# Kernel tuning notes

Hardware: AMD Instinct MI355X
Metric: run time of the kernel (lower is better)

The kernel has to match this reference:

```python
import jax, jax.numpy as jnp
import numpy as np

N_SAMPLES = 4194304
N_RAYS = 131072


def setup_inputs() -> dict:
    key = jax.random.key(0)
    k1, k2, k3, k4, k5, k6 = jax.random.split(key, 6)
    alpha = jax.random.uniform(k1, (N_SAMPLES, 1), dtype=jnp.float32)
    values3d = jax.random.uniform(k2, (N_SAMPLES, 3), dtype=jnp.float32)
    values1d = jax.random.uniform(k3, (N_SAMPLES, 1), dtype=jnp.float32)
    weights = jax.random.uniform(k4, (N_SAMPLES, 1), dtype=jnp.float32)
    sample_values = jax.random.normal(k5, (N_SAMPLES, 3), dtype=jnp.float32)
    ray_id = jnp.sort(jax.random.randint(k6, (N_SAMPLES,), 0, N_RAYS, dtype=jnp.int32))
    return {"alpha": alpha, "values3d": values3d, "values1d": values1d,
            "weights": weights, "sample_values": sample_values,
            "ray_id": ray_id, "n_rays": N_RAYS}


def _transmittance(alpha, ray_id, n_rays):
    # exclusive cumprod of (1 - alpha) within each packed ray segment, in log space
    logs = jnp.log(jnp.clip(1.0 - alpha[:, 0], 1e-7, 1.0))          # [N]
    csum = jnp.cumsum(logs)
    excl = csum - logs                                               # exclusive cumsum
    first = jnp.concatenate([jnp.ones((1,), bool), ray_id[1:] != ray_id[:-1]])
    seg_base = jax.ops.segment_sum(jnp.where(first, excl, 0.0), ray_id,
                                   num_segments=n_rays)              # [R]
    transmittance = jnp.exp(excl - seg_base[ray_id])[:, None]        # [N,1]
    bg_transmittance = jnp.exp(jax.ops.segment_sum(logs, ray_id,
                                                   num_segments=n_rays))  # [R]
    return transmittance, bg_transmittance


def reference(alpha, values3d, values1d, weights, sample_values, ray_id, n_rays):
    transmittance, bg_transmittance = _transmittance(alpha, ray_id, n_rays)
    # integrate_3d / integrate_1d: per-ray sum of value * weight
    integrated_3d = jax.ops.segment_sum(values3d * weights, ray_id, num_segments=n_rays)  # [R,3]
    integrated_1d = jax.ops.segment_sum(values1d * weights, ray_id, num_segments=n_rays)  # [R,1]
    # SumOverRay: per-ray sum plus broadcast back to each sample
    sum_per_ray = jax.ops.segment_sum(sample_values, ray_id, num_segments=n_rays)         # [R,3]
    sum_per_sample = sum_per_ray[ray_id]                                                  # [N,3]
    return (transmittance, bg_transmittance, integrated_3d, integrated_1d,
            sum_per_ray, sum_per_sample)
```

## Files before the change

### kernel.cpp

```cpp
#include <hip/hip_runtime.h>

typedef float f32x4 __attribute__((ext_vector_type(4)));

template<int CTRL>
__device__ __forceinline__ float dpp1(float x) {
    return __int_as_float(__builtin_amdgcn_update_dpp(
        0x3f800000, __float_as_int(x), CTRL, 0xF, 0xF, false));
}
template<int CTRL>
__device__ __forceinline__ float dpp0(float x) {
    return __int_as_float(__builtin_amdgcn_update_dpp(
        0, __float_as_int(x), CTRL, 0xF, 0xF, true));
}
template<int PAT>
__device__ __forceinline__ float swz(float x) {
    return __int_as_float(__builtin_amdgcn_ds_swizzle(__float_as_int(x), PAT));
}
#define FUNNEL16(v) do { \
    v += dpp0<0x111>(v); \
    v += dpp0<0x112>(v); \
    v += dpp0<0x114>(v); \
    v += dpp0<0x118>(v); } while (0)

__device__ __forceinline__ void ntst4(float* p, float x, float y, float z, float w) {
    f32x4 v = {x, y, z, w};
    __builtin_nontemporal_store(v, (f32x4*)p);
}

__global__ __launch_bounds__(256) void seg_bounds_kernel(
    const int* __restrict__ ray_id, int n, int* __restrict__ seg_se)
{
    const int t = blockIdx.x * blockDim.x + threadIdx.x;
    const int a = t * 4;
    if (a >= n) return;
    const int4 rv = *(const int4*)(ray_id + a);
    const int prev = (a == 0) ? -1 : ray_id[a - 1];
    const int nxt  = (a + 4 < n) ? ray_id[a + 4] : -1;

    if (rv.x != prev) seg_se[2 * rv.x] = a;
    if (rv.y != rv.x) { seg_se[2 * rv.x + 1] = a + 1; seg_se[2 * rv.y] = a + 1; }
    if (rv.z != rv.y) { seg_se[2 * rv.y + 1] = a + 2; seg_se[2 * rv.z] = a + 2; }
    if (rv.w != rv.z) { seg_se[2 * rv.z + 1] = a + 3; seg_se[2 * rv.w] = a + 3; }
    if (rv.w != nxt)  seg_se[2 * rv.w + 1] = a + 4;
}

__global__ __launch_bounds__(256) void ray_kernel(
    const float* __restrict__ alpha,
    const float* __restrict__ values3d,
    const float* __restrict__ values1d,
    const float* __restrict__ weights,
    const float* __restrict__ sample_values,
    const int*   __restrict__ ray_id,
    const int*   __restrict__ seg_se,
    float* __restrict__ out_T,
    float* __restrict__ out_bg,
    float* __restrict__ out_i3,
    float* __restrict__ out_i1,
    float* __restrict__ out_spr,
    float* __restrict__ out_sps,
    int R, int N)
{
    __shared__ float prr[16][8];

    const int lane = threadIdx.x & 63;
    const int wid  = threadIdx.x >> 6;
    const int j    = lane & 15;
    const int g    = lane >> 4;
    const int slot = wid * 4 + g;
    const int r0   = blockIdx.x * 16;
    const int r    = r0 + slot;
    const bool ray_ok = (r < R);
    const int rc = ray_ok ? r : 0;

    const int2 se = ((const int2*)seg_se)[rc];
    int s0 = se.x, s1 = se.y;
    const bool arith = ray_ok & (s0 >= 0) & (s0 < s1) & (s1 <= N);
    if (!arith) { s0 = 0; s1 = 0; }

    const int chk = ray_id[s0];
    const bool valid = arith & (chk == rc);

    float c = 1.0f;
    float i3x = 0.f, i3y = 0.f, i3z = 0.f, i1 = 0.f;
    float sx = 0.f, sy = 0.f, sz = 0.f;

    const int base0 = s0 & ~3;

    for (int base = base0; base < s1; base += 64) {
        const int a = base + 4 * j;
        const bool tile_ok = (a < s1);
        const int  al = tile_ok ? a : base0;

        const f32x4 av  = *(const f32x4*)(alpha + al);
        const f32x4 wv  = *(const f32x4*)(weights + al);
        const f32x4 v1v = *(const f32x4*)(values1d + al);
        const f32x4 b0  = *(const f32x4*)(values3d + 3 * al);
        const f32x4 b1  = *(const f32x4*)(values3d + 3 * al + 4);
        const f32x4 b2  = *(const f32x4*)(values3d + 3 * al + 8);
        const f32x4 q0  = *(const f32x4*)(sample_values + 3 * al);
        const f32x4 q1  = *(const f32x4*)(sample_values + 3 * al + 4);
        const f32x4 q2  = *(const f32x4*)(sample_values + 3 * al + 8);

        const bool w0 = valid & tile_ok & (a + 0 >= s0);
        const bool w1 = valid & tile_ok & (a + 1 >= s0) & (a + 1 < s1);
        const bool w2 = valid & tile_ok & (a + 2 >= s0) & (a + 2 < s1);
        const bool w3 = valid & tile_ok & (a + 3 < s1);

        float o0 = fminf(fmaxf(1.0f - av.x, 1e-7f), 1.0f); if (!w0) o0 = 1.0f;
        float o1 = fminf(fmaxf(1.0f - av.y, 1e-7f), 1.0f); if (!w1) o1 = 1.0f;
        float o2 = fminf(fmaxf(1.0f - av.z, 1e-7f), 1.0f); if (!w2) o2 = 1.0f;
        float o3 = fminf(fmaxf(1.0f - av.w, 1e-7f), 1.0f); if (!w3) o3 = 1.0f;

        const float p01  = o0 * o1;
        const float p012 = p01 * o2;
        float p = p012 * o3;

        p *= dpp1<0x111>(p);
        p *= dpp1<0x112>(p);
        p *= dpp1<0x114>(p);
        p *= dpp1<0x118>(p);
        const float gincl = p;
        const float gexcl = dpp1<0x111>(gincl);

        const float cg = c * gexcl;
        const float t0 = cg;
        const float t1 = cg * o0;
        const float t2 = cg * p01;
        const float t3 = cg * p012;

        const float W0 = w0 ? wv.x : 0.f;
        const float W1 = w1 ? wv.y : 0.f;
        const float W2 = w2 ? wv.z : 0.f;
        const float W3 = w3 ? wv.w : 0.f;
        const float M0 = w0 ? 1.f : 0.f;
        const float M1 = w1 ? 1.f : 0.f;
        const float M2 = w2 ? 1.f : 0.f;
        const float M3 = w3 ? 1.f : 0.f;

        i1  += v1v.x * W0 + v1v.y * W1 + v1v.z * W2 + v1v.w * W3;
        i3x += b0.x * W0 + b0.w * W1 + b1.z * W2 + b2.y * W3;
        i3y += b0.y * W0 + b1.x * W1 + b1.w * W2 + b2.z * W3;
        i3z += b0.z * W0 + b1.y * W1 + b2.x * W2 + b2.w * W3;
        sx  += q0.x * M0 + q0.w * M1 + q1.z * M2 + q2.y * M3;
        sy  += q0.y * M0 + q1.x * M1 + q1.w * M2 + q2.z * M3;
        sz  += q0.z * M0 + q1.y * M1 + q2.x * M2 + q2.w * M3;

        if (w0 & w1 & w2 & w3) {
            ntst4(out_T + a, t0, t1, t2, t3);
        } else {
            if (w0) out_T[a + 0] = t0;
            if (w1) out_T[a + 1] = t1;
            if (w2) out_T[a + 2] = t2;
            if (w3) out_T[a + 3] = t3;
        }

        c *= swz<0x1F0>(gincl);
    }

    FUNNEL16(i3x); FUNNEL16(i3y); FUNNEL16(i3z); FUNNEL16(i1);
    FUNNEL16(sx);  FUNNEL16(sy);  FUNNEL16(sz);
    sx = swz<0x1F0>(sx);
    sy = swz<0x1F0>(sy);
    sz = swz<0x1F0>(sz);

    if (j == 15) {
        prr[slot][0] = c;
        prr[slot][1] = i1;
        prr[slot][2] = i3x; prr[slot][3] = i3y; prr[slot][4] = i3z;
        prr[slot][5] = sx;  prr[slot][6] = sy;  prr[slot][7] = sz;
    }
    __syncthreads();

    {
        const int t = threadIdx.x;
        if (t < 128) {
            float val; float* addr; int ridx;
            if (t < 16)      { ridx = t;            val = prr[ridx][0];          addr = out_bg  + r0 + t; }
            else if (t < 32) { ridx = t - 16;       val = prr[ridx][1];          addr = out_i1  + r0 + ridx; }
            else if (t < 80) { int s = t - 32; ridx = s / 3; val = prr[ridx][2 + s % 3]; addr = out_i3  + 3 * r0 + s; }
            else             { int s = t - 80; ridx = s / 3; val = prr[ridx][5 + s % 3]; addr = out_spr + 3 * r0 + s; }
            if (r0 + ridx < R) *addr = val;
        }
    }

    for (int base = base0; base < s1; base += 64) {
        const int a = base + 4 * j;
        const bool tile_ok = (a < s1);
        const bool w0 = valid & tile_ok & (a + 0 >= s0);
        const bool w1 = valid & tile_ok & (a + 1 >= s0) & (a + 1 < s1);
        const bool w2 = valid & tile_ok & (a + 2 >= s0) & (a + 2 < s1);
        const bool w3 = valid & tile_ok & (a + 3 < s1);
        if (w0 & w1 & w2 & w3) {
            ntst4(out_sps + 3 * a,     sx, sy, sz, sx);
            ntst4(out_sps + 3 * a + 4, sy, sz, sx, sy);
            ntst4(out_sps + 3 * a + 8, sz, sx, sy, sz);
        } else {
            if (w0) { out_sps[3*a+0] = sx; out_sps[3*a+1]  = sy; out_sps[3*a+2]  = sz; }
            if (w1) { out_sps[3*a+3] = sx; out_sps[3*a+4]  = sy; out_sps[3*a+5]  = sz; }
            if (w2) { out_sps[3*a+6] = sx; out_sps[3*a+7]  = sy; out_sps[3*a+8]  = sz; }
            if (w3) { out_sps[3*a+9] = sx; out_sps[3*a+10] = sy; out_sps[3*a+11] = sz; }
        }
    }
}

extern "C" void kernel_launch(void* const* d_in, const int* in_sizes, int n_in,
                              void* d_out, int out_size, void* d_ws, size_t ws_size,
                              hipStream_t stream) {
    const float* alpha = (const float*)d_in[0];
    const float* v3    = (const float*)d_in[1];
    const float* v1    = (const float*)d_in[2];
    const float* w     = (const float*)d_in[3];
    const float* sv    = (const float*)d_in[4];
    const int*   rid   = (const int*)d_in[5];

    int N = in_sizes[0];
    int R = (out_size - 4 * N) / 8;

    int* seg_se = (int*)d_ws;

    float* out     = (float*)d_out;
    float* out_T   = out;
    float* out_bg  = out + N;
    float* out_i3  = out_bg + R;
    float* out_i1  = out_i3 + 3 * (size_t)R;
    float* out_spr = out_i1 + R;
    float* out_sps = out_spr + 3 * (size_t)R;

    const int nquad = N / 4;
    seg_bounds_kernel<<<(nquad + 255) / 256, 256, 0, stream>>>(rid, N, seg_se);

    int blocks = (R + 15) / 16;
    ray_kernel<<<blocks, 256, 0, stream>>>(alpha, v3, v1, w, sv, rid, seg_se,
                                           out_T, out_bg, out_i3, out_i1, out_spr,
                                           out_sps, R, N);
}
```

Before: 48.78 us.

## Fill empty-ray bounds in seg kernel and write per-sample sums as aligned flat vectors

The segment-bounds kernel now also writes start/end entries for rays with no samples, including the ranges before the first and after the last ray. This removes the validity check and the extra ray_id gather from the ray kernel. The per-sample broadcast store now runs over the flat 3*N float range with 16-byte aligned nontemporal vector stores and scalar head and tail pieces, instead of per-quad masked stores. The bounds kernel may now loop over runs of empty ray ids. The prr shared array is padded from 8 to 9 floats per row.

```diff
diff --git a/kernel.cpp b/kernel.cpp
--- a/kernel.cpp
+++ b/kernel.cpp
@@ -26,22 +26,35 @@
     f32x4 v = {x, y, z, w};
     __builtin_nontemporal_store(v, (f32x4*)p);
 }
+__device__ __forceinline__ float sel3(int m, float x, float y, float z) {
+    return m == 0 ? x : (m == 1 ? y : z);
+}
 
 __global__ __launch_bounds__(256) void seg_bounds_kernel(
-    const int* __restrict__ ray_id, int n, int* __restrict__ seg_se)
+    const int* __restrict__ ray_id, int n, int R, int* __restrict__ seg_se)
 {
     const int t = blockIdx.x * blockDim.x + threadIdx.x;
     const int a = t * 4;
     if (a >= n) return;
     const int4 rv = *(const int4*)(ray_id + a);
-    const int prev = (a == 0) ? -1 : ray_id[a - 1];
-    const int nxt  = (a + 4 < n) ? ray_id[a + 4] : -1;
-
-    if (rv.x != prev) seg_se[2 * rv.x] = a;
-    if (rv.y != rv.x) { seg_se[2 * rv.x + 1] = a + 1; seg_se[2 * rv.y] = a + 1; }
-    if (rv.z != rv.y) { seg_se[2 * rv.y + 1] = a + 2; seg_se[2 * rv.z] = a + 2; }
-    if (rv.w != rv.z) { seg_se[2 * rv.z + 1] = a + 3; seg_se[2 * rv.w] = a + 3; }
-    if (rv.w != nxt)  seg_se[2 * rv.w + 1] = a + 4;
+
+#define TRANS(u, v, p) do {                                                   \
+        if ((u) >= 0) seg_se[2 * (u) + 1] = (p);                              \
+        for (int id_ = (u) + 1; id_ < (v); ++id_) {                           \
+            seg_se[2 * id_] = (p); seg_se[2 * id_ + 1] = (p); }               \
+        if ((v) < R) seg_se[2 * (v)] = (p); } while (0)
+
+    if (a == 0) TRANS(-1, rv.x, 0);
+    if (rv.y != rv.x) TRANS(rv.x, rv.y, a + 1);
+    if (rv.z != rv.y) TRANS(rv.y, rv.z, a + 2);
+    if (rv.w != rv.z) TRANS(rv.z, rv.w, a + 3);
+    if (a + 4 == n) {
+        TRANS(rv.w, R, n);
+    } else {
+        const int nx = ray_id[a + 4];
+        if (nx != rv.w) TRANS(rv.w, nx, a + 4);
+    }
+#undef TRANS
 }
 
 __global__ __launch_bounds__(256) void ray_kernel(
@@ -50,7 +63,6 @@
     const float* __restrict__ values1d,
     const float* __restrict__ weights,
     const float* __restrict__ sample_values,
-    const int*   __restrict__ ray_id,
     const int*   __restrict__ seg_se,
     float* __restrict__ out_T,
     float* __restrict__ out_bg,
@@ -58,9 +70,9 @@
     float* __restrict__ out_i1,
     float* __restrict__ out_spr,
     float* __restrict__ out_sps,
-    int R, int N)
+    int R)
 {
-    __shared__ float prr[16][8];
+    __shared__ float prr[16][9];
 
     const int lane = threadIdx.x & 63;
     const int wid  = threadIdx.x >> 6;
@@ -74,11 +86,7 @@
 
     const int2 se = ((const int2*)seg_se)[rc];
     int s0 = se.x, s1 = se.y;
-    const bool arith = ray_ok & (s0 >= 0) & (s0 < s1) & (s1 <= N);
-    if (!arith) { s0 = 0; s1 = 0; }
-
-    const int chk = ray_id[s0];
-    const bool valid = arith & (chk == rc);
+    if (!ray_ok) { s0 = 0; s1 = 0; }
 
     float c = 1.0f;
     float i3x = 0.f, i3y = 0.f, i3z = 0.f, i1 = 0.f;
@@ -101,10 +109,10 @@
         const f32x4 q1  = *(const f32x4*)(sample_values + 3 * al + 4);
         const f32x4 q2  = *(const f32x4*)(sample_values + 3 * al + 8);
 
-        const bool w0 = valid & tile_ok & (a + 0 >= s0);
-        const bool w1 = valid & tile_ok & (a + 1 >= s0) & (a + 1 < s1);
-        const bool w2 = valid & tile_ok & (a + 2 >= s0) & (a + 2 < s1);
-        const bool w3 = valid & tile_ok & (a + 3 < s1);
+        const bool w0 = tile_ok & (a + 0 >= s0);
+        const bool w1 = tile_ok & (a + 1 >= s0) & (a + 1 < s1);
+        const bool w2 = tile_ok & (a + 2 >= s0) & (a + 2 < s1);
+        const bool w3 = tile_ok & (a + 3 < s1);
 
         float o0 = fminf(fmaxf(1.0f - av.x, 1e-7f), 1.0f); if (!w0) o0 = 1.0f;
         float o1 = fminf(fmaxf(1.0f - av.y, 1e-7f), 1.0f); if (!w1) o1 = 1.0f;
@@ -183,22 +191,18 @@
         }
     }
 
-    for (int base = base0; base < s1; base += 64) {
-        const int a = base + 4 * j;
-        const bool tile_ok = (a < s1);
-        const bool w0 = valid & tile_ok & (a + 0 >= s0);
-        const bool w1 = valid & tile_ok & (a + 1 >= s0) & (a + 1 < s1);
-        const bool w2 = valid & tile_ok & (a + 2 >= s0) & (a + 2 < s1);
-        const bool w3 = valid & tile_ok & (a + 3 < s1);
-        if (w0 & w1 & w2 & w3) {
-            ntst4(out_sps + 3 * a,     sx, sy, sz, sx);
-            ntst4(out_sps + 3 * a + 4, sy, sz, sx, sy);
-            ntst4(out_sps + 3 * a + 8, sz, sx, sy, sz);
-        } else {
-            if (w0) { out_sps[3*a+0] = sx; out_sps[3*a+1]  = sy; out_sps[3*a+2]  = sz; }
-            if (w1) { out_sps[3*a+3] = sx; out_sps[3*a+4]  = sy; out_sps[3*a+5]  = sz; }
-            if (w2) { out_sps[3*a+6] = sx; out_sps[3*a+7]  = sy; out_sps[3*a+8]  = sz; }
-            if (w3) { out_sps[3*a+9] = sx; out_sps[3*a+10] = sy; out_sps[3*a+11] = sz; }
+    {
+        const int F0 = 3 * s0, F1 = 3 * s1;
+        const int H1 = min((F0 + 3) & ~3, F1);
+        const int A1 = max(F1 & ~3, H1);
+        if (j == 0) for (int f = F0; f < H1; ++f) out_sps[f] = sel3(f % 3, sx, sy, sz);
+        if (j == 1) for (int f = A1; f < F1; ++f) out_sps[f] = sel3(f % 3, sx, sy, sz);
+        for (int f = H1 + 4 * j; f < A1; f += 64) {
+            const int m = f % 3;
+            const float v0 = sel3(m, sx, sy, sz);
+            const float v1 = sel3(m == 2 ? 0 : m + 1, sx, sy, sz);
+            const float v2 = sel3(m == 0 ? 2 : m - 1, sx, sy, sz);
+            ntst4(out_sps + f, v0, v1, v2, v0);
         }
     }
 }
@@ -227,10 +231,10 @@
     float* out_sps = out_spr + 3 * (size_t)R;
 
     const int nquad = N / 4;
-    seg_bounds_kernel<<<(nquad + 255) / 256, 256, 0, stream>>>(rid, N, seg_se);
+    seg_bounds_kernel<<<(nquad + 255) / 256, 256, 0, stream>>>(rid, N, R, seg_se);
 
     int blocks = (R + 15) / 16;
-    ray_kernel<<<blocks, 256, 0, stream>>>(alpha, v3, v1, w, sv, rid, seg_se,
+    ray_kernel<<<blocks, 256, 0, stream>>>(alpha, v3, v1, w, sv, seg_se,
                                            out_T, out_bg, out_i3, out_i1, out_spr,
-                                           out_sps, R, N);
-}
+                                           out_sps, R);
+}
```

After: 45.92 us. -5.9%, faster.
